# Performance work log

Measured on AMD Instinct MI355X. Metric: run time of the kernel, lower is better.

The kernel has to match this reference:

```python
import jax, jax.numpy as jnp
import numpy as np

N_NODES = 40000


def _gcn_conv(x, edge_index, W, b):
    """PyG GCNConv: add self-loops, symmetric degree normalization,
    linear transform, gather-scale-scatter aggregation, bias."""
    n = x.shape[0]
    loops = jnp.arange(n, dtype=edge_index.dtype)
    src = jnp.concatenate([edge_index[0], loops])  # [E+N]
    dst = jnp.concatenate([edge_index[1], loops])  # [E+N]
    ones = jnp.ones(src.shape[0], dtype=x.dtype)
    deg = jax.ops.segment_sum(ones, dst, num_segments=n)  # in-degree incl. self-loop
    dinv = jnp.where(deg > 0, jax.lax.rsqrt(deg), 0.0)
    norm = dinv[src] * dinv[dst]  # [E+N]
    h = x @ W  # [n, out]
    msg = h[src] * norm[:, None]  # [E+N, out] gather + scale
    out = jax.ops.segment_sum(msg, dst, num_segments=n)  # scatter-add
    return out + b


def setup_inputs() -> dict:
    key = jax.random.key(0)
    k = jax.random.split(key, 6)
    n, din, dh, dout = N_NODES, 128, 128, 64
    x = jax.random.normal(k[0], (n, din), dtype=jnp.float32)
    edge_index = jax.random.randint(k[1], (2, 640000), 0, n, dtype=jnp.int64)
    W1 = jax.random.normal(k[2], (din, dh), dtype=jnp.float32) / np.sqrt(din)
    b1 = jnp.zeros((dh,), dtype=jnp.float32)
    W2 = jax.random.normal(k[3], (dh, dout), dtype=jnp.float32) / np.sqrt(dh)
    b2 = jnp.zeros((dout,), dtype=jnp.float32)
    return {"x": x, "edge_index": edge_index, "W1": W1, "b1": b1, "W2": W2, "b2": b2}


def reference(x, edge_index, W1, b1, W2, b2):
    h = jax.nn.relu(_gcn_conv(x, edge_index, W1, b1))
    return _gcn_conv(h, edge_index, W2, b2)
```

## Files before the change

### kernel.cpp

```cpp
#include <hip/hip_runtime.h>
#include <hip/hip_fp16.h>


#define N_NODES 40000
#define DIN 128
#define DH 128
#define DOUT 64
#define NEDGES 640000
#define CAP 64
#define NBUCKET 2560
#define I4_PER_CHUNK 500
#define NODES_PER_XCD 5000
#define NCVT 1250

typedef _Float16 f16x8 __attribute__((ext_vector_type(8)));
typedef float f32x4 __attribute__((ext_vector_type(4)));

__global__ void k_init(int* __restrict__ deg, const float* __restrict__ W1,
                       const float* __restrict__ W2,
                       _Float16* __restrict__ WT1, _Float16* __restrict__ WT2, int n) {
    int i = blockIdx.x * 256 + threadIdx.x;
    if (i < n) deg[i] = 0;
    if (i < DIN * DH) {
        int k = i >> 7, nn = i & 127;
        WT1[(size_t)nn * DIN + k] = (_Float16)W1[i];
    }
    if (i < DH * DOUT) {
        int k = i >> 6, nn = i & 63;
        WT2[(size_t)nn * DH + k] = (_Float16)W2[i];
    }
}

__global__ __launch_bounds__(256) void k_bkt_cvt(
    const float* __restrict__ x, _Float16* __restrict__ xh,
    const int4* __restrict__ src4, const int4* __restrict__ dst4,
    int* __restrict__ deg, unsigned short* __restrict__ ssrc)
{
    if (blockIdx.x < NBUCKET) {
        const int xg = blockIdx.x & 7;
        const int c  = blockIdx.x >> 3;
        const int lo = xg * NODES_PER_XCD, hi = lo + NODES_PER_XCD;
        const int e0 = c * I4_PER_CHUNK, e1 = e0 + I4_PER_CHUNK;
        for (int e = e0 + threadIdx.x; e < e1; e += 256) {
            int4 d = dst4[e];
            int4 s = src4[e];
            if (d.x >= lo && d.x < hi) {
                int p = atomicAdd(&deg[d.x], 1);
                if (p < CAP) ssrc[d.x * CAP + p] = (unsigned short)s.x;
            }
            if (d.y >= lo && d.y < hi) {
                int p = atomicAdd(&deg[d.y], 1);
                if (p < CAP) ssrc[d.y * CAP + p] = (unsigned short)s.y;
            }
            if (d.z >= lo && d.z < hi) {
                int p = atomicAdd(&deg[d.z], 1);
                if (p < CAP) ssrc[d.z * CAP + p] = (unsigned short)s.z;
            }
            if (d.w >= lo && d.w < hi) {
                int p = atomicAdd(&deg[d.w], 1);
                if (p < CAP) ssrc[d.w * CAP + p] = (unsigned short)s.w;
            }
        }
    } else {
        const size_t base = ((size_t)(blockIdx.x - NBUCKET) * 256 + threadIdx.x) * 16;
        float4 a0 = *(const float4*)(x + base);
        float4 a1 = *(const float4*)(x + base + 4);
        float4 a2 = *(const float4*)(x + base + 8);
        float4 a3 = *(const float4*)(x + base + 12);
        f16x8 o0 = { (_Float16)a0.x, (_Float16)a0.y, (_Float16)a0.z, (_Float16)a0.w,
                     (_Float16)a1.x, (_Float16)a1.y, (_Float16)a1.z, (_Float16)a1.w };
        f16x8 o1 = { (_Float16)a2.x, (_Float16)a2.y, (_Float16)a2.z, (_Float16)a2.w,
                     (_Float16)a3.x, (_Float16)a3.y, (_Float16)a3.z, (_Float16)a3.w };
        *(f16x8*)(xh + base)     = o0;
        *(f16x8*)(xh + base + 8) = o1;
    }
}

__global__ __launch_bounds__(1024) void k_agg_g12(
    const int* __restrict__ deg, const unsigned short* __restrict__ ssrc,
    const __half* __restrict__ xh, const float* __restrict__ b1,
    const _Float16* __restrict__ WT1, const _Float16* __restrict__ WT2,
    __half* __restrict__ h2)
{
    __shared__ _Float16 ys[16][136];
    __shared__ _Float16 zs[16][136];
    const int w = threadIdx.x >> 6;
    const int lane = threadIdx.x & 63;
    const int node0 = blockIdx.x * 16;
    const int node = node0 + w;
    const __half2* hp = (const __half2*)xh;

    const int dg = deg[node];
    const int cnt = min(dg, CAP);
    const float dn = rsqrtf((float)(dg + 1));
    float2 self = __half22float2(hp[(size_t)node * 64 + lane]);
    float2 acc = { self.x * dn, self.y * dn };
    int sv = (lane < cnt) ? (int)ssrc[node * CAP + lane] : 0;
    float dval = (lane < cnt) ? rsqrtf((float)(deg[sv] + 1)) : 0.f;
    int e = 0;
    for (; e + 8 <= cnt; e += 8) {
        int s0 = __shfl(sv, e),     s1 = __shfl(sv, e + 1);
        int s2 = __shfl(sv, e + 2), s3 = __shfl(sv, e + 3);
        int s4 = __shfl(sv, e + 4), s5 = __shfl(sv, e + 5);
        int s6 = __shfl(sv, e + 6), s7 = __shfl(sv, e + 7);
        float w0 = __shfl(dval, e),     w1 = __shfl(dval, e + 1);
        float w2 = __shfl(dval, e + 2), w3 = __shfl(dval, e + 3);
        float w4 = __shfl(dval, e + 4), w5 = __shfl(dval, e + 5);
        float w6 = __shfl(dval, e + 6), w7 = __shfl(dval, e + 7);
        float2 v0 = __half22float2(hp[(size_t)s0 * 64 + lane]);
        float2 v1 = __half22float2(hp[(size_t)s1 * 64 + lane]);
        float2 v2 = __half22float2(hp[(size_t)s2 * 64 + lane]);
        float2 v3 = __half22float2(hp[(size_t)s3 * 64 + lane]);
        float2 v4 = __half22float2(hp[(size_t)s4 * 64 + lane]);
        float2 v5 = __half22float2(hp[(size_t)s5 * 64 + lane]);
        float2 v6 = __half22float2(hp[(size_t)s6 * 64 + lane]);
        float2 v7 = __half22float2(hp[(size_t)s7 * 64 + lane]);
        acc.x += (v0.x * w0 + v1.x * w1) + (v2.x * w2 + v3.x * w3)
               + (v4.x * w4 + v5.x * w5) + (v6.x * w6 + v7.x * w7);
        acc.y += (v0.y * w0 + v1.y * w1) + (v2.y * w2 + v3.y * w3)
               + (v4.y * w4 + v5.y * w5) + (v6.y * w6 + v7.y * w7);
    }
    for (; e < cnt; ++e) {
        int s = __shfl(sv, e);
        float wv = __shfl(dval, e);
        float2 v = __half22float2(hp[(size_t)s * 64 + lane]);
        acc.x += v.x * wv; acc.y += v.y * wv;
    }
    ys[w][2 * lane]     = (_Float16)(dn * acc.x);
    ys[w][2 * lane + 1] = (_Float16)(dn * acc.y);
    __syncthreads();

    const int m = lane & 15, quad = lane >> 4;
    if (w < 8) {
        f32x4 acc1 = (f32x4){0.f, 0.f, 0.f, 0.f};
#pragma unroll
        for (int ks = 0; ks < 4; ++ks) {
            f16x8 a = *(const f16x8*)&ys[m][ks * 32 + quad * 8];
            f16x8 b = *(const f16x8*)(WT1 + (size_t)(w * 16 + m) * DIN + ks * 32 + quad * 8);
            acc1 = __builtin_amdgcn_mfma_f32_16x16x32_f16(a, b, acc1, 0, 0, 0);
        }
        float bias = b1[w * 16 + m];
#pragma unroll
        for (int r = 0; r < 4; ++r) {
            float v = acc1[r] + bias;
            zs[quad * 4 + r][w * 16 + m] = (_Float16)(v > 0.f ? v : 0.f);
        }
    }
    __syncthreads();

    if (w < 4) {
        f32x4 acc2 = (f32x4){0.f, 0.f, 0.f, 0.f};
#pragma unroll
        for (int ks = 0; ks < 4; ++ks) {
            f16x8 a = *(const f16x8*)&zs[m][ks * 32 + quad * 8];
            f16x8 b = *(const f16x8*)(WT2 + (size_t)(w * 16 + m) * DH + ks * 32 + quad * 8);
            acc2 = __builtin_amdgcn_mfma_f32_16x16x32_f16(a, b, acc2, 0, 0, 0);
        }
#pragma unroll
        for (int r = 0; r < 4; ++r) {
            int nrow = node0 + quad * 4 + r;
            float dnr = rsqrtf((float)(deg[nrow] + 1));
            h2[(size_t)nrow * DOUT + w * 16 + m] = (__half)(acc2[r] * dnr);
        }
    }
}

__global__ __launch_bounds__(256) void k_agg2(
    const int* __restrict__ deg, const unsigned short* __restrict__ ssrc,
    const __half* __restrict__ h, const float* __restrict__ b2,
    float* __restrict__ out)
{
    const int node = blockIdx.x * 4 + (threadIdx.x >> 6);
    const int lane = threadIdx.x & 63;
    const int half = lane >> 5;
    const int lp = lane & 31;
    const int dg = deg[node];
    const int cnt = min(dg, CAP);
    const __half2* hp = (const __half2*)h;

    float2 acc;
    if (half == 0) acc = __half22float2(hp[(size_t)node * 32 + lp]);
    else           acc = make_float2(0.f, 0.f);

    int sv = (lane < cnt) ? (int)ssrc[node * CAP + lane] : 0;
    int e = 0;
    for (; e + 16 <= cnt; e += 16) {
        int b = e + half;
        int s0 = __shfl(sv, b),      s1 = __shfl(sv, b + 2);
        int s2 = __shfl(sv, b + 4),  s3 = __shfl(sv, b + 6);
        int s4 = __shfl(sv, b + 8),  s5 = __shfl(sv, b + 10);
        int s6 = __shfl(sv, b + 12), s7 = __shfl(sv, b + 14);
        float2 v0 = __half22float2(hp[(size_t)s0 * 32 + lp]);
        float2 v1 = __half22float2(hp[(size_t)s1 * 32 + lp]);
        float2 v2 = __half22float2(hp[(size_t)s2 * 32 + lp]);
        float2 v3 = __half22float2(hp[(size_t)s3 * 32 + lp]);
        float2 v4 = __half22float2(hp[(size_t)s4 * 32 + lp]);
        float2 v5 = __half22float2(hp[(size_t)s5 * 32 + lp]);
        float2 v6 = __half22float2(hp[(size_t)s6 * 32 + lp]);
        float2 v7 = __half22float2(hp[(size_t)s7 * 32 + lp]);
        acc.x += ((v0.x + v1.x) + (v2.x + v3.x)) + ((v4.x + v5.x) + (v6.x + v7.x));
        acc.y += ((v0.y + v1.y) + (v2.y + v3.y)) + ((v4.y + v5.y) + (v6.y + v7.y));
    }
    for (; e + 2 <= cnt; e += 2) {
        int s = __shfl(sv, e + half);
        float2 v = __half22float2(hp[(size_t)s * 32 + lp]);
        acc.x += v.x; acc.y += v.y;
    }
    if (e < cnt) {
        int s = __shfl(sv, e);
        if (half == 0) {
            float2 v = __half22float2(hp[(size_t)s * 32 + lp]);
            acc.x += v.x; acc.y += v.y;
        }
    }
    acc.x += __shfl_xor(acc.x, 32);
    acc.y += __shfl_xor(acc.y, 32);
    if (half == 0) {
        float dn = rsqrtf((float)(dg + 1));
        float2 o;
        o.x = dn * acc.x + b2[2 * lp];
        o.y = dn * acc.y + b2[2 * lp + 1];
        *(float2*)&out[(size_t)node * 64 + 2 * lp] = o;
    }
}

extern "C" void kernel_launch(void* const* d_in, const int* in_sizes, int n_in,
                              void* d_out, int out_size, void* d_ws, size_t ws_size,
                              hipStream_t stream) {
    const float* x  = (const float*)d_in[0];
    const int*   ei = (const int*)d_in[1];
    const float* W1 = (const float*)d_in[2];
    const float* b1 = (const float*)d_in[3];
    const float* W2 = (const float*)d_in[4];
    const float* b2 = (const float*)d_in[5];
    float* out = (float*)d_out;

    const int n = N_NODES, E = NEDGES;
    const int* src = ei;
    const int* dst = ei + E;

    char* ws = (char*)d_ws;
    int*            deg  = (int*)(ws + 0);
    _Float16*       WT1  = (_Float16*)(ws + 163840);
    _Float16*       WT2  = (_Float16*)(ws + 196608);
    unsigned short* ssrc = (unsigned short*)(ws + 212992);
    _Float16*       xh   = (_Float16*)(ws + 5332992);
    __half*         h2   = (__half*)(ws + 15572992);

    k_init    <<<(n + 255) / 256, 256, 0, stream>>>(deg, W1, W2, WT1, WT2, n);
    k_bkt_cvt <<<NBUCKET + NCVT, 256, 0, stream>>>(x, xh, (const int4*)src,
                                                   (const int4*)dst, deg, ssrc);
    k_agg_g12 <<<n / 16, 1024, 0, stream>>>(deg, ssrc, (const __half*)xh, b1,
                                            WT1, WT2, h2);
    k_agg2    <<<n / 4,  256, 0, stream>>>(deg, ssrc, h2, b2, out);
}
```

Measured before the change: 171.9 us.

## Fold weight transpose into bucket kernel; read neighbor ids as packed uint4

Drops the k_init kernel. The degree array is now zeroed with hipMemsetAsync, and the W1/W2 fp16 transpose runs in extra blocks of the bucketing kernel, so there is one less launch. In both aggregation kernels, the per-wave cooperative load of neighbor ids plus shuffle broadcast is replaced by uniform uint4 loads of 8 packed ushort ids, and per-neighbor degree weights are computed inline. This removes shuffles but adds redundant scalar/broadcast deg loads and rsqrt work per lane.

```diff
diff --git a/kernel.cpp b/kernel.cpp
--- a/kernel.cpp
+++ b/kernel.cpp
@@ -12,29 +12,17 @@
 #define I4_PER_CHUNK 500
 #define NODES_PER_XCD 5000
 #define NCVT 1250
+#define NWT 8
 
 typedef _Float16 f16x8 __attribute__((ext_vector_type(8)));
 typedef float f32x4 __attribute__((ext_vector_type(4)));
-
-__global__ void k_init(int* __restrict__ deg, const float* __restrict__ W1,
-                       const float* __restrict__ W2,
-                       _Float16* __restrict__ WT1, _Float16* __restrict__ WT2, int n) {
-    int i = blockIdx.x * 256 + threadIdx.x;
-    if (i < n) deg[i] = 0;
-    if (i < DIN * DH) {
-        int k = i >> 7, nn = i & 127;
-        WT1[(size_t)nn * DIN + k] = (_Float16)W1[i];
-    }
-    if (i < DH * DOUT) {
-        int k = i >> 6, nn = i & 63;
-        WT2[(size_t)nn * DH + k] = (_Float16)W2[i];
-    }
-}
 
 __global__ __launch_bounds__(256) void k_bkt_cvt(
     const float* __restrict__ x, _Float16* __restrict__ xh,
     const int4* __restrict__ src4, const int4* __restrict__ dst4,
-    int* __restrict__ deg, unsigned short* __restrict__ ssrc)
+    int* __restrict__ deg, unsigned short* __restrict__ ssrc,
+    const float* __restrict__ W1, const float* __restrict__ W2,
+    _Float16* __restrict__ WT1, _Float16* __restrict__ WT2)
 {
     if (blockIdx.x < NBUCKET) {
         const int xg = blockIdx.x & 7;
@@ -61,7 +49,7 @@
                 if (p < CAP) ssrc[d.w * CAP + p] = (unsigned short)s.w;
             }
         }
-    } else {
+    } else if (blockIdx.x < NBUCKET + NCVT) {
         const size_t base = ((size_t)(blockIdx.x - NBUCKET) * 256 + threadIdx.x) * 16;
         float4 a0 = *(const float4*)(x + base);
         float4 a1 = *(const float4*)(x + base + 4);
@@ -73,6 +61,16 @@
                      (_Float16)a3.x, (_Float16)a3.y, (_Float16)a3.z, (_Float16)a3.w };
         *(f16x8*)(xh + base)     = o0;
         *(f16x8*)(xh + base + 8) = o1;
+    } else {
+        const int b = blockIdx.x - NBUCKET - NCVT;
+        for (int i = b * 256 + threadIdx.x; i < DIN * DH; i += NWT * 256) {
+            int k = i >> 7, nn = i & 127;
+            WT1[nn * DIN + k] = (_Float16)W1[i];
+        }
+        for (int i = b * 256 + threadIdx.x; i < DH * DOUT; i += NWT * 256) {
+            int k = i >> 6, nn = i & 63;
+            WT2[nn * DH + k] = (_Float16)W2[i];
+        }
     }
 }
 
@@ -95,18 +93,18 @@
     const float dn = rsqrtf((float)(dg + 1));
     float2 self = __half22float2(hp[(size_t)node * 64 + lane]);
     float2 acc = { self.x * dn, self.y * dn };
-    int sv = (lane < cnt) ? (int)ssrc[node * CAP + lane] : 0;
-    float dval = (lane < cnt) ? rsqrtf((float)(deg[sv] + 1)) : 0.f;
+    const uint4* bin4 = (const uint4*)(ssrc + (size_t)node * CAP);
     int e = 0;
     for (; e + 8 <= cnt; e += 8) {
-        int s0 = __shfl(sv, e),     s1 = __shfl(sv, e + 1);
-        int s2 = __shfl(sv, e + 2), s3 = __shfl(sv, e + 3);
-        int s4 = __shfl(sv, e + 4), s5 = __shfl(sv, e + 5);
-        int s6 = __shfl(sv, e + 6), s7 = __shfl(sv, e + 7);
-        float w0 = __shfl(dval, e),     w1 = __shfl(dval, e + 1);
-        float w2 = __shfl(dval, e + 2), w3 = __shfl(dval, e + 3);
-        float w4 = __shfl(dval, e + 4), w5 = __shfl(dval, e + 5);
-        float w6 = __shfl(dval, e + 6), w7 = __shfl(dval, e + 7);
+        uint4 pk = bin4[e >> 3];
+        int s0 = pk.x & 0xFFFF, s1 = pk.x >> 16;
+        int s2 = pk.y & 0xFFFF, s3 = pk.y >> 16;
+        int s4 = pk.z & 0xFFFF, s5 = pk.z >> 16;
+        int s6 = pk.w & 0xFFFF, s7 = pk.w >> 16;
+        float w0 = rsqrtf((float)(deg[s0] + 1)), w1 = rsqrtf((float)(deg[s1] + 1));
+        float w2 = rsqrtf((float)(deg[s2] + 1)), w3 = rsqrtf((float)(deg[s3] + 1));
+        float w4 = rsqrtf((float)(deg[s4] + 1)), w5 = rsqrtf((float)(deg[s5] + 1));
+        float w6 = rsqrtf((float)(deg[s6] + 1)), w7 = rsqrtf((float)(deg[s7] + 1));
         float2 v0 = __half22float2(hp[(size_t)s0 * 64 + lane]);
         float2 v1 = __half22float2(hp[(size_t)s1 * 64 + lane]);
         float2 v2 = __half22float2(hp[(size_t)s2 * 64 + lane]);
@@ -121,8 +119,8 @@
                + (v4.y * w4 + v5.y * w5) + (v6.y * w6 + v7.y * w7);
     }
     for (; e < cnt; ++e) {
-        int s = __shfl(sv, e);
-        float wv = __shfl(dval, e);
+        int s = ssrc[(size_t)node * CAP + e];
+        float wv = rsqrtf((float)(deg[s] + 1));
         float2 v = __half22float2(hp[(size_t)s * 64 + lane]);
         acc.x += v.x * wv; acc.y += v.y * wv;
     }
@@ -182,32 +180,29 @@
     if (half == 0) acc = __half22float2(hp[(size_t)node * 32 + lp]);
     else           acc = make_float2(0.f, 0.f);
 
-    int sv = (lane < cnt) ? (int)ssrc[node * CAP + lane] : 0;
+    const uint4* bin4 = (const uint4*)(ssrc + (size_t)node * CAP);
     int e = 0;
-    for (; e + 16 <= cnt; e += 16) {
-        int b = e + half;
-        int s0 = __shfl(sv, b),      s1 = __shfl(sv, b + 2);
-        int s2 = __shfl(sv, b + 4),  s3 = __shfl(sv, b + 6);
-        int s4 = __shfl(sv, b + 8),  s5 = __shfl(sv, b + 10);
-        int s6 = __shfl(sv, b + 12), s7 = __shfl(sv, b + 14);
-        float2 v0 = __half22float2(hp[(size_t)s0 * 32 + lp]);
-        float2 v1 = __half22float2(hp[(size_t)s1 * 32 + lp]);
-        float2 v2 = __half22float2(hp[(size_t)s2 * 32 + lp]);
-        float2 v3 = __half22float2(hp[(size_t)s3 * 32 + lp]);
-        float2 v4 = __half22float2(hp[(size_t)s4 * 32 + lp]);
-        float2 v5 = __half22float2(hp[(size_t)s5 * 32 + lp]);
-        float2 v6 = __half22float2(hp[(size_t)s6 * 32 + lp]);
-        float2 v7 = __half22float2(hp[(size_t)s7 * 32 + lp]);
-        acc.x += ((v0.x + v1.x) + (v2.x + v3.x)) + ((v4.x + v5.x) + (v6.x + v7.x));
-        acc.y += ((v0.y + v1.y) + (v2.y + v3.y)) + ((v4.y + v5.y) + (v6.y + v7.y));
+    for (; e + 8 <= cnt; e += 8) {
+        uint4 pk = bin4[e >> 3];
+        int sa, sb, sc, sd;
+        if (half == 0) { sa = pk.x & 0xFFFF; sb = pk.y & 0xFFFF;
+                         sc = pk.z & 0xFFFF; sd = pk.w & 0xFFFF; }
+        else           { sa = pk.x >> 16;    sb = pk.y >> 16;
+                         sc = pk.z >> 16;    sd = pk.w >> 16; }
+        float2 v0 = __half22float2(hp[(size_t)sa * 32 + lp]);
+        float2 v1 = __half22float2(hp[(size_t)sb * 32 + lp]);
+        float2 v2 = __half22float2(hp[(size_t)sc * 32 + lp]);
+        float2 v3 = __half22float2(hp[(size_t)sd * 32 + lp]);
+        acc.x += (v0.x + v1.x) + (v2.x + v3.x);
+        acc.y += (v0.y + v1.y) + (v2.y + v3.y);
     }
     for (; e + 2 <= cnt; e += 2) {
-        int s = __shfl(sv, e + half);
+        int s = ssrc[(size_t)node * CAP + e + half];
         float2 v = __half22float2(hp[(size_t)s * 32 + lp]);
         acc.x += v.x; acc.y += v.y;
     }
     if (e < cnt) {
-        int s = __shfl(sv, e);
+        int s = ssrc[(size_t)node * CAP + e];
         if (half == 0) {
             float2 v = __half22float2(hp[(size_t)s * 32 + lp]);
             acc.x += v.x; acc.y += v.y;
@@ -247,9 +242,10 @@
     _Float16*       xh   = (_Float16*)(ws + 5332992);
     __half*         h2   = (__half*)(ws + 15572992);
 
-    k_init    <<<(n + 255) / 256, 256, 0, stream>>>(deg, W1, W2, WT1, WT2, n);
-    k_bkt_cvt <<<NBUCKET + NCVT, 256, 0, stream>>>(x, xh, (const int4*)src,
-                                                   (const int4*)dst, deg, ssrc);
+    hipMemsetAsync(deg, 0, N_NODES * sizeof(int), stream);
+    k_bkt_cvt <<<NBUCKET + NCVT + NWT, 256, 0, stream>>>(x, xh, (const int4*)src,
+                                                         (const int4*)dst, deg, ssrc,
+                                                         W1, W2, WT1, WT2);
     k_agg_g12 <<<n / 16, 1024, 0, stream>>>(deg, ssrc, (const __half*)xh, b1,
                                             WT1, WT2, h2);
     k_agg2    <<<n / 4,  256, 0, stream>>>(deg, ssrc, h2, b2, out);
```

New measurement: 181.0 us. +5.3%, slower.
